# Optimization experiments

Hardware: AMD Instinct MI355X
Metric: run time of the kernel (lower is better)

Reference implementation:

```python
import jax, jax.numpy as jnp
import numpy as np

N_NODES = 100000
N_EDGES = 600000
N_GRAPHS = 64
EPS = 1e-5


def setup_inputs() -> dict:
    key = jax.random.key(0)
    ks = jax.random.split(key, 8)
    x = jax.random.normal(ks[0], (N_NODES, 128), dtype=jnp.float32)
    edge_index = jax.random.randint(ks[1], (2, N_EDGES), 0, N_NODES, dtype=jnp.int64)
    batch = jnp.sort(jax.random.randint(ks[2], (N_NODES,), 0, N_GRAPHS, dtype=jnp.int64))
    conv_w = jax.random.normal(ks[3], (6, 128, 128), dtype=jnp.float32) * (1.0 / np.sqrt(128))
    conv_b = jnp.zeros((6, 128), dtype=jnp.float32)
    bn_g = jnp.ones((6, 128), dtype=jnp.float32)
    bn_b = jnp.zeros((6, 128), dtype=jnp.float32)
    lin1_w = jax.random.normal(ks[4], (128, 64), dtype=jnp.float32) * (1.0 / np.sqrt(128))
    lin1_b = jnp.zeros((64,), dtype=jnp.float32)
    lin2_w = jax.random.normal(ks[5], (64, 4), dtype=jnp.float32) * (1.0 / np.sqrt(64))
    lin2_b = jnp.zeros((4,), dtype=jnp.float32)
    return {"x": x, "edge_index": edge_index, "batch": batch,
            "conv_w": conv_w, "conv_b": conv_b, "bn_g": bn_g, "bn_b": bn_b,
            "lin1_w": lin1_w, "lin1_b": lin1_b, "lin2_w": lin2_w, "lin2_b": lin2_b}


def reference(x, edge_index, batch, conv_w, conv_b, bn_g, bn_b, lin1_w, lin1_b, lin2_w, lin2_b):
    src, dst = edge_index[0], edge_index[1]  # messages flow src -> dst (PyG source_to_target)
    n = x.shape[0]
    h = x
    # 6 stacked GCNConv(normalize=False) -> ReLU -> BatchNorm1d (training-mode batch stats)
    for i in range(6):
        m = h @ conv_w[i]                                   # [N, H] transform first
        agg = jax.ops.segment_sum(m[src], dst, num_segments=n) + conv_b[i]
        h = jax.nn.relu(agg)
        mean = h.mean(axis=0)
        var = h.var(axis=0)                                  # biased, matches torch BN
        h = (h - mean) * jax.lax.rsqrt(var + EPS) * bn_g[i] + bn_b[i]
    # global mean pool over graphs
    s = jax.ops.segment_sum(h, batch, num_segments=N_GRAPHS)          # [G, H]
    cnt = jax.ops.segment_sum(jnp.ones((n,), h.dtype), batch, num_segments=N_GRAPHS)
    pooled = s / jnp.maximum(cnt, 1.0)[:, None]
    out = pooled @ lin1_w + lin1_b
    out = out @ lin2_w + lin2_b
    return jax.nn.log_softmax(out, axis=-1)
```

## Files before the change

### kernel.cpp

```cpp
#include <hip/hip_runtime.h>
#include <math.h>

#define NN 100000
#define NE 600000
#define NG 64
#define HD 128
#define NL 6
#define NB 1563
#define PSL 16
#define ASTR 136
#define CASTB 12500
#define EBL 2344
#define RSTR 379

typedef unsigned short ushort_t;
typedef short short8 __attribute__((ext_vector_type(8)));
typedef float floatx4 __attribute__((ext_vector_type(4)));

__device__ __forceinline__ float bf2f(ushort_t u) {
    return __uint_as_float(((unsigned)u) << 16);
}
__device__ __forceinline__ ushort_t f2bf(float f) {
    unsigned u = __float_as_uint(f);
    unsigned r = (u + 0x7fffu + ((u >> 16) & 1u)) >> 16;
    return (ushort_t)r;
}


__global__ __launch_bounds__(256) void k_prep(const float* __restrict__ x,
                                              ushort_t* __restrict__ xb,
                                              const float* __restrict__ W,
                                              ushort_t* __restrict__ Wt,
                                              ushort_t* __restrict__ hb0,
                                              ushort_t* __restrict__ hb1,
                                              const int* __restrict__ ei,
                                              int* __restrict__ counts) {
    int bid = blockIdx.x;
    if (bid < CASTB) {
        int i = bid * 256 + threadIdx.x;
        float4 v = ((const float4*)x)[i];
        ((ushort4*)xb)[i] = make_ushort4(f2bf(v.x), f2bf(v.y), f2bf(v.z), f2bf(v.w));
    } else if (bid < CASTB + NL) {
        const float* Wl = W + (size_t)(bid - CASTB) * 16384;
        ushort_t* Wtl = Wt + (size_t)(bid - CASTB) * 16384;
        for (int id = threadIdx.x; id < 16384; id += 256) {
            int k = id >> 7, c = id & 127;
            Wtl[c * 128 + k] = f2bf(Wl[id]);
        }
        if (bid == CASTB && threadIdx.x < 96) {
            int t = threadIdx.x;
            ushort_t* base = (t < 32) ? xb : ((t < 64) ? hb0 : hb1);
            *(ushort4*)(base + (size_t)NN * 128 + (size_t)(t & 31) * 4) =
                make_ushort4(0, 0, 0, 0);
        }
    } else {
        int e = (bid - CASTB - NL) * 256 + threadIdx.x;
        if (e < NE) atomicAdd(&counts[ei[NE + e]], 1);
    }
}


__global__ __launch_bounds__(256) void k_scan1(const int* __restrict__ counts, int* __restrict__ bsums) {
    __shared__ int s[256];
    int i = blockIdx.x * 256 + threadIdx.x;
    s[threadIdx.x] = (i < NN) ? counts[i] : 0;
    __syncthreads();
    for (int off = 128; off > 0; off >>= 1) {
        if (threadIdx.x < off) s[threadIdx.x] += s[threadIdx.x + off];
        __syncthreads();
    }
    if (threadIdx.x == 0) bsums[blockIdx.x] = s[0];
}

__global__ __launch_bounds__(256) void k_scan3m(const int* __restrict__ counts,
                                                const int* __restrict__ bsums,
                                                int* __restrict__ rowptr) {
    __shared__ int s[256];
    int t = threadIdx.x;
    int i = blockIdx.x * 256 + t;
    int v = (i < NN) ? counts[i] : 0;
    s[t] = v;
    __syncthreads();
    for (int off = 1; off < 256; off <<= 1) {
        int u = (t >= off) ? s[t - off] : 0;
        __syncthreads();
        s[t] += u;
        __syncthreads();
    }
    int incl = s[t];
    int pb = 0;
    for (int j = t; j < blockIdx.x; j += 256) pb += bsums[j];
    __syncthreads();
    s[t] = pb;
    __syncthreads();
    for (int off = 128; off > 0; off >>= 1) {
        if (t < off) s[t] += s[t + off];
        __syncthreads();
    }
    int base = s[0];
    if (i < NN) rowptr[i] = base + incl - v;
    if (i == 0) rowptr[NN] = NE;
}

__global__ __launch_bounds__(256) void k_filldh(const int* __restrict__ ei,
                                                const int* __restrict__ rowptr,
                                                int* __restrict__ cursor,
                                                int* __restrict__ colsrc,
                                                int* __restrict__ dcount,
                                                int ebl) {
    int t = threadIdx.x;
    if ((int)blockIdx.x < ebl) {
        int e = blockIdx.x * 256 + t;
        if (e < NE) {
            int d = ei[NE + e];
            int pos = rowptr[d] + atomicAdd(&cursor[d], 1);
            colsrc[pos] = ei[e];
        }
    } else {
        __shared__ int lc[64];
        if (t < 64) lc[t] = 0;
        __syncthreads();
        int n = (blockIdx.x - ebl) * 256 + t;
        if (n < NN) {
            int d = rowptr[n + 1] - rowptr[n];
            atomicAdd(&lc[min(d, 63)], 1);
        }
        __syncthreads();
        if (t < 64 && lc[t] > 0) atomicAdd(&dcount[t], lc[t]);
    }
}

__global__ __launch_bounds__(256) void k_dfill2(const int* __restrict__ rowptr,
                                                const int* __restrict__ dcount,
                                                int* __restrict__ dcursor,
                                                int* __restrict__ perm) {
    __shared__ int lc[64], lbase[64], doffs[64];
    int t = threadIdx.x;
    if (t < 64) {
        lc[t] = 0;
        int s = 0;
        for (int b = t + 1; b < 64; ++b) s += dcount[b];
        doffs[t] = s;
    }
    __syncthreads();
    int n = blockIdx.x * 256 + t;
    int b = 0, my = 0;
    if (n < NN) {
        int d = rowptr[n + 1] - rowptr[n];
        b = min(d, 63);
        my = atomicAdd(&lc[b], 1);
    }
    __syncthreads();
    if (t < 64 && lc[t] > 0) lbase[t] = atomicAdd(&dcursor[t], lc[t]);
    __syncthreads();
    if (n < NN) perm[doffs[b] + lbase[b] + my] = n;
}


__global__ __launch_bounds__(256, 4) void k_gconv(
    const ushort_t* __restrict__ hin, const int* __restrict__ perm,
    const int* __restrict__ rowptr, const int* __restrict__ colsrc,
    const float* __restrict__ stats_in, const float* __restrict__ bng,
    const float* __restrict__ bnb,
    const ushort_t* __restrict__ Wt, const float* __restrict__ bias,
    ushort_t* __restrict__ hout, float* __restrict__ partials) {
    __shared__ ushort_t Ab[64 * ASTR];
    __shared__ float sstat[256];
    int t = threadIdx.x;
    sstat[t] = 0.f;
    __syncthreads();
    int wave = t >> 6, lane = t & 63;
    int l15 = lane & 15, quad = lane >> 4;
    int l5 = lane & 31, half = lane >> 5;
    int rank = (RSTR * blockIdx.x) % NB;
    int rowbase = rank * 64 + wave * 16;

    int idxg = rowbase + l15;
    bool vr = idxg < NN;
    int prm = vr ? perm[idxg] : 0;
    int rb = vr ? rowptr[prm] : 0;
    int re = vr ? rowptr[prm + 1] : 0;
    int dg = re - rb;

    int f0 = l5 * 4;
    float sc[4] = {1.f, 1.f, 1.f, 1.f}, sh[4] = {0.f, 0.f, 0.f, 0.f};
    if (stats_in != nullptr) {
        const float inv_n = 1.0f / (float)NN;
        float4 s1 = *(const float4*)&stats_in[f0];
        float4 s2 = *(const float4*)&stats_in[HD + f0];
        float4 g4 = *(const float4*)&bng[f0];
        float4 b4 = *(const float4*)&bnb[f0];
        float m, var;
        m = s1.x * inv_n; var = fmaf(-m, m, s2.x * inv_n);
        sc[0] = g4.x * rsqrtf(var + 1e-5f); sh[0] = b4.x - m * sc[0];
        m = s1.y * inv_n; var = fmaf(-m, m, s2.y * inv_n);
        sc[1] = g4.y * rsqrtf(var + 1e-5f); sh[1] = b4.y - m * sc[1];
        m = s1.z * inv_n; var = fmaf(-m, m, s2.z * inv_n);
        sc[2] = g4.z * rsqrtf(var + 1e-5f); sh[2] = b4.z - m * sc[2];
        m = s1.w * inv_n; var = fmaf(-m, m, s2.w * inv_n);
        sc[3] = g4.w * rsqrtf(var + 1e-5f); sh[3] = b4.w - m * sc[3];
    }

    const uint2* hbl = (const uint2*)hin + l5;

    int b0 = __shfl(rb, half, 64);
    int d0 = __shfl(dg, half, 64);
    int b1 = __shfl(rb, 2 + half, 64);
    int d1 = __shfl(dg, 2 + half, 64);
    int cs0[4], cs1[4];
    #pragma unroll
    for (int eo = 0; eo < 4; ++eo) {
        int c0 = colsrc[b0 + eo];
        int c1 = colsrc[b1 + eo];
        cs0[eo] = (eo < d0) ? c0 : NN;
        cs1[eo] = (eo < d1) ? c1 : NN;
    }

    #pragma unroll 1
    for (int g = 0; g < 4; ++g) {
        int mx = max(d0, d1);
        mx = max(mx, __shfl_xor(mx, 32, 64));

        float a0[4] = {0.f, 0.f, 0.f, 0.f};
        float a1[4] = {0.f, 0.f, 0.f, 0.f};

        #pragma unroll 1
        for (int e = 0; e < mx; e += 4) {
            uint2 hv0[4], hv1[4];
            #pragma unroll
            for (int eo = 0; eo < 4; ++eo) hv0[eo] = hbl[(size_t)cs0[eo] * 32];
            #pragma unroll
            for (int eo = 0; eo < 4; ++eo) hv1[eo] = hbl[(size_t)cs1[eo] * 32];
            int nc0[4], nc1[4];
            #pragma unroll
            for (int eo = 0; eo < 4; ++eo) {
                int e4 = e + 4 + eo;
                int c0 = colsrc[b0 + e4];
                int c1 = colsrc[b1 + e4];
                nc0[eo] = (e4 < d0) ? c0 : NN;
                nc1[eo] = (e4 < d1) ? c1 : NN;
            }
            #pragma unroll
            for (int eo = 0; eo < 4; ++eo) {
                unsigned wx = hv0[eo].x, wy = hv0[eo].y;
                a0[0] += __uint_as_float(wx << 16);
                a0[1] += __uint_as_float(wx & 0xffff0000u);
                a0[2] += __uint_as_float(wy << 16);
                a0[3] += __uint_as_float(wy & 0xffff0000u);
                unsigned zx = hv1[eo].x, zy = hv1[eo].y;
                a1[0] += __uint_as_float(zx << 16);
                a1[1] += __uint_as_float(zx & 0xffff0000u);
                a1[2] += __uint_as_float(zy << 16);
                a1[3] += __uint_as_float(zy & 0xffff0000u);
            }
            #pragma unroll
            for (int eo = 0; eo < 4; ++eo) { cs0[eo] = nc0[eo]; cs1[eo] = nc1[eo]; }
        }

        int nb0 = 0, nd0 = 0, nb1 = 0, nd1 = 0;
        if (g < 3) {
            int t0 = (g + 1) * 4 + half, t1 = t0 + 2;
            nb0 = __shfl(rb, t0, 64);
            nd0 = __shfl(dg, t0, 64);
            nb1 = __shfl(rb, t1, 64);
            nd1 = __shfl(dg, t1, 64);
            #pragma unroll
            for (int eo = 0; eo < 4; ++eo) {
                int c0 = colsrc[nb0 + eo];
                int c1 = colsrc[nb1 + eo];
                cs0[eo] = (eo < nd0) ? c0 : NN;
                cs1[eo] = (eo < nd1) ? c1 : NN;
            }
        }

        float df0 = (float)d0, df1 = (float)d1;
        ushort4 u0, u1;
        u0.x = f2bf(fmaf(sc[0], a0[0], df0 * sh[0]));
        u0.y = f2bf(fmaf(sc[1], a0[1], df0 * sh[1]));
        u0.z = f2bf(fmaf(sc[2], a0[2], df0 * sh[2]));
        u0.w = f2bf(fmaf(sc[3], a0[3], df0 * sh[3]));
        u1.x = f2bf(fmaf(sc[0], a1[0], df1 * sh[0]));
        u1.y = f2bf(fmaf(sc[1], a1[1], df1 * sh[1]));
        u1.z = f2bf(fmaf(sc[2], a1[2], df1 * sh[2]));
        u1.w = f2bf(fmaf(sc[3], a1[3], df1 * sh[3]));
        *(ushort4*)&Ab[(wave * 16 + g * 4 + half) * ASTR + f0] = u0;
        *(ushort4*)&Ab[(wave * 16 + g * 4 + 2 + half) * ASTR + f0] = u1;

        b0 = nb0; d0 = nd0; b1 = nb1; d1 = nd1;
    }

    short8 afrag[4];
    #pragma unroll
    for (int s = 0; s < 4; ++s)
        afrag[s] = *(const short8*)&Ab[(wave * 16 + l15) * ASTR + quad * 8 + s * 32];

    floatx4 acc[8];
    #pragma unroll
    for (int c = 0; c < 8; ++c) acc[c] = (floatx4){0.f, 0.f, 0.f, 0.f};
    #pragma unroll
    for (int c = 0; c < 8; ++c) {
        size_t boff = (size_t)(16 * c + l15) * 128 + quad * 8;
        #pragma unroll
        for (int s = 0; s < 4; ++s) {
            short8 bf = *(const short8*)(Wt + boff + 32 * s);
            acc[c] = __builtin_amdgcn_mfma_f32_16x16x32_bf16(afrag[s], bf, acc[c], 0, 0, 0);
        }
    }

    int orow0 = rowbase + quad * 4;
    #pragma unroll
    for (int c = 0; c < 8; ++c) {
        int col = 16 * c + l15;
        float bv = bias[col];
        float ls = 0.f, lq = 0.f;
        #pragma unroll
        for (int i = 0; i < 4; ++i) {
            float v = fmaxf(acc[c][i] + bv, 0.f);
            ushort_t bb = f2bf(v);
            Ab[(wave * 16 + quad * 4 + i) * ASTR + col] = bb;
            if (orow0 + i < NN) {
                float vr2 = bf2f(bb);
                ls += vr2;
                lq = fmaf(vr2, vr2, lq);
            }
        }
        ls += __shfl_xor(ls, 16, 64);
        ls += __shfl_xor(ls, 32, 64);
        lq += __shfl_xor(lq, 16, 64);
        lq += __shfl_xor(lq, 32, 64);
        if (quad == 0) {
            atomicAdd(&sstat[col], ls);
            atomicAdd(&sstat[128 + col], lq);
        }
    }

    #pragma unroll
    for (int it = 0; it < 4; ++it) {
        int pr = __shfl(prm, it * 4 + quad, 64);
        int ridx = rowbase + it * 4 + quad;
        if (ridx < NN) {
            short8 v = *(const short8*)&Ab[(wave * 16 + it * 4 + quad) * ASTR + l15 * 8];
            *(short8*)(hout + (size_t)pr * 128 + l15 * 8) = v;
        }
    }

    __syncthreads();
    partials[(size_t)blockIdx.x * 256 + t] = sstat[t];
}


__global__ __launch_bounds__(256) void k_red(const float* __restrict__ partials,
                                             float* __restrict__ stats) {
    int t = threadIdx.x;
    float s = 0.f;
    for (int r = blockIdx.x; r < NB; r += 64) s += partials[(size_t)r * 256 + t];
    atomicAdd(&stats[t], s);
}


__device__ __forceinline__ int lowerb(const int* __restrict__ b, int n, int key) {
    int lo = 0, hi = n;
    while (lo < hi) {
        int mid = (lo + hi) >> 1;
        if (b[mid] < key) lo = mid + 1;
        else hi = mid;
    }
    return lo;
}

__global__ __launch_bounds__(256) void k_pool1(
    const ushort_t* __restrict__ h, const int* __restrict__ batch,
    float* __restrict__ ppart) {
    int g = blockIdx.x >> 4;
    int sl = blockIdx.x & (PSL - 1);
    int lo = lowerb(batch, NN, g);
    int hi = lowerb(batch, NN, g + 1);
    int cnt = hi - lo;
    int a = lo + (int)(((long long)cnt * sl) >> 4);
    int b = lo + (int)(((long long)cnt * (sl + 1)) >> 4);
    int wave = threadIdx.x >> 6, lane = threadIdx.x & 63;
    const ushort2* h2 = (const ushort2*)h;
    float ax = 0.f, ay = 0.f;
    for (int n = a + wave; n < b; n += 4) {
        ushort2 v = h2[(size_t)n * 64 + lane];
        ax += bf2f(v.x);
        ay += bf2f(v.y);
    }
    __shared__ float2 red[4][64];
    red[wave][lane] = make_float2(ax, ay);
    __syncthreads();
    if (wave == 0) {
        float sx = 0.f, sy = 0.f;
        for (int w = 0; w < 4; ++w) {
            sx += red[w][lane].x;
            sy += red[w][lane].y;
        }
        ((float2*)ppart)[(size_t)blockIdx.x * 64 + lane] = make_float2(sx, sy);
    }
}


__global__ __launch_bounds__(64) void k_tail(
    const float* __restrict__ ppart, const int* __restrict__ batch,
    const float* __restrict__ stats, const float* __restrict__ bng, const float* __restrict__ bnb,
    const float* __restrict__ w1, const float* __restrict__ b1,
    const float* __restrict__ w2, const float* __restrict__ b2,
    float* __restrict__ out) {
    __shared__ float p[128];
    int g = blockIdx.x;
    int lane = threadIdx.x;
    float sx = 0.f, sy = 0.f;
    #pragma unroll
    for (int s = 0; s < PSL; ++s) {
        float2 v = ((const float2*)ppart)[(size_t)(g * PSL + s) * 64 + lane];
        sx += v.x;
        sy += v.y;
    }
    int cnt = lowerb(batch, NN, g + 1) - lowerb(batch, NN, g);
    int c0 = lane * 2;
    const float inv_n = 1.0f / (float)NN;
    float m0 = stats[c0] * inv_n, m1 = stats[c0 + 1] * inv_n;
    float var0 = fmaf(-m0, m0, stats[HD + c0] * inv_n);
    float var1 = fmaf(-m1, m1, stats[HD + c0 + 1] * inv_n);
    float sc0 = bng[c0] * rsqrtf(var0 + 1e-5f);
    float sc1 = bng[c0 + 1] * rsqrtf(var1 + 1e-5f);
    float sh0 = bnb[c0] - m0 * sc0;
    float sh1 = bnb[c0 + 1] - m1 * sc1;
    float denom = fmaxf((float)cnt, 1.f);
    p[c0] = (sc0 * sx + (float)cnt * sh0) / denom;
    p[c0 + 1] = (sc1 * sy + (float)cnt * sh1) / denom;
    __syncthreads();

    float hid = b1[lane];
    #pragma unroll 8
    for (int k = 0; k < 128; ++k) hid = fmaf(p[k], w1[k * 64 + lane], hid);
    float o[4];
    #pragma unroll
    for (int c = 0; c < 4; ++c) {
        float v = hid * w2[lane * 4 + c];
        #pragma unroll
        for (int off = 1; off < 64; off <<= 1) v += __shfl_xor(v, off, 64);
        o[c] = v + b2[c];
    }
    if (lane == 0) {
        float mx = fmaxf(fmaxf(o[0], o[1]), fmaxf(o[2], o[3]));
        float se = expf(o[0] - mx) + expf(o[1] - mx) + expf(o[2] - mx) + expf(o[3] - mx);
        float ls = mx + logf(se);
        #pragma unroll
        for (int c = 0; c < 4; ++c) out[g * 4 + c] = o[c] - ls;
    }
}

extern "C" void kernel_launch(void* const* d_in, const int* in_sizes, int n_in,
                              void* d_out, int out_size, void* d_ws, size_t ws_size,
                              hipStream_t stream) {
    const float* x = (const float*)d_in[0];
    const int* ei = (const int*)d_in[1];
    const int* batch = (const int*)d_in[2];
    const float* conv_w = (const float*)d_in[3];
    const float* conv_b = (const float*)d_in[4];
    const float* bn_g = (const float*)d_in[5];
    const float* bn_b = (const float*)d_in[6];
    const float* l1w = (const float*)d_in[7];
    const float* l1b = (const float*)d_in[8];
    const float* l2w = (const float*)d_in[9];
    const float* l2b = (const float*)d_in[10];
    float* out = (float*)d_out;
    (void)in_sizes; (void)n_in; (void)out_size; (void)ws_size;

    char* ws = (char*)d_ws;
    int* counts = (int*)(ws + 0);
    int* cursor = (int*)(ws + 400000);
    int* perm = (int*)(ws + 400000);
    float* stats = (float*)(ws + 800000);
    int* dcount = (int*)(ws + 806144);
    int* dcursor = (int*)(ws + 806400);
    const size_t zero_bytes = 806656;
    int* rowptr = (int*)(ws + 806656);
    int* bsums = (int*)(ws + 1206664);
    int* colsrc = (int*)(ws + 1208256);
    float* ppart = (float*)(ws + 3609280);
    float* partials = (float*)(ws + 4133568);
    ushort_t* xb = (ushort_t*)(ws + 5734144);
    ushort_t* hb0 = (ushort_t*)(ws + 31334400);
    ushort_t* hb1 = (ushort_t*)(ws + 56934656);
    ushort_t* wtbuf = (ushort_t*)(ws + 82534912);

    hipMemsetAsync(ws, 0, zero_bytes, stream);

    k_prep<<<CASTB + NL + EBL, 256, 0, stream>>>(x, xb, conv_w, wtbuf, hb0, hb1, ei, counts);

    int nb1 = (NN + 255) / 256;
    k_scan1<<<nb1, 256, 0, stream>>>(counts, bsums);
    k_scan3m<<<nb1, 256, 0, stream>>>(counts, bsums, rowptr);
    k_filldh<<<EBL + nb1, 256, 0, stream>>>(ei, rowptr, cursor, colsrc, dcount, EBL);
    k_dfill2<<<nb1, 256, 0, stream>>>(rowptr, dcount, dcursor, perm);

    ushort_t* hb[2] = {hb0, hb1};
    for (int L = 0; L < NL; ++L) {
        const ushort_t* hin = (L == 0) ? xb : hb[(L + 1) & 1];
        ushort_t* hout = hb[L & 1];
        const float* lstats = (L == 0) ? nullptr : (stats + (L - 1) * 256);
        const float* lg = (L == 0) ? nullptr : (bn_g + (L - 1) * 128);
        const float* lb = (L == 0) ? nullptr : (bn_b + (L - 1) * 128);
        k_gconv<<<NB, 256, 0, stream>>>(hin, perm, rowptr, colsrc, lstats, lg, lb,
                                        wtbuf + L * 16384, conv_b + L * 128,
                                        hout, partials);
        k_red<<<64, 256, 0, stream>>>(partials, stats + L * 256);
    }
    k_pool1<<<NG * PSL, 256, 0, stream>>>(hb1, batch, ppart);
    k_tail<<<NG, 64, 0, stream>>>(ppart, batch, stats + 5 * 256, bn_g + 5 * 128, bn_b + 5 * 128,
                                  l1w, l1b, l2w, l2b, out);
}
```

Measured before the change: 642.0 us.

## Store intermediate layer features in degree-sorted order with remapped edge sources

Layers 0-4 now write their output rows in permuted (degree-sorted) row order, so each block writes one contiguous range instead of scattering rows through perm. A new kernel builds an inverse permutation and remaps the edge source indices so later layers gather from the permuted layout. The last layer writes back in original order for pooling. This adds one small remap kernel and an extra index array, and the gathers become permuted-space accesses that may have different locality.

Result: no change. 653.0 us (+1.7%).

```diff
diff --git a/kernel.cpp b/kernel.cpp
--- a/kernel.cpp
+++ b/kernel.cpp
@@ -133,7 +133,8 @@
 __global__ __launch_bounds__(256) void k_dfill2(const int* __restrict__ rowptr,
                                                 const int* __restrict__ dcount,
                                                 int* __restrict__ dcursor,
-                                                int* __restrict__ perm) {
+                                                int* __restrict__ perm,
+                                                int* __restrict__ inv_perm) {
     __shared__ int lc[64], lbase[64], doffs[64];
     int t = threadIdx.x;
     if (t < 64) {
@@ -153,7 +154,18 @@
     __syncthreads();
     if (t < 64 && lc[t] > 0) lbase[t] = atomicAdd(&dcursor[t], lc[t]);
     __syncthreads();
-    if (n < NN) perm[doffs[b] + lbase[b] + my] = n;
+    if (n < NN) {
+        int r = doffs[b] + lbase[b] + my;
+        perm[r] = n;
+        inv_perm[n] = r;
+    }
+}
+
+__global__ __launch_bounds__(256) void k_trans(const int* __restrict__ colsrc,
+                                               const int* __restrict__ inv_perm,
+                                               int* __restrict__ colsrc_s) {
+    int e = blockIdx.x * 256 + threadIdx.x;
+    if (e < NE) colsrc_s[e] = inv_perm[colsrc[e]];
 }
 
 
@@ -163,7 +175,8 @@
     const float* __restrict__ stats_in, const float* __restrict__ bng,
     const float* __restrict__ bnb,
     const ushort_t* __restrict__ Wt, const float* __restrict__ bias,
-    ushort_t* __restrict__ hout, float* __restrict__ partials) {
+    ushort_t* __restrict__ hout, float* __restrict__ partials,
+    const int store_orig) {
     __shared__ ushort_t Ab[64 * ASTR];
     __shared__ float sstat[256];
     int t = threadIdx.x;
@@ -336,11 +349,12 @@
 
     #pragma unroll
     for (int it = 0; it < 4; ++it) {
+        int ridx = rowbase + it * 4 + quad;
         int pr = __shfl(prm, it * 4 + quad, 64);
-        int ridx = rowbase + it * 4 + quad;
+        int trg = store_orig ? pr : ridx;
         if (ridx < NN) {
             short8 v = *(const short8*)&Ab[(wave * 16 + it * 4 + quad) * ASTR + l15 * 8];
-            *(short8*)(hout + (size_t)pr * 128 + l15 * 8) = v;
+            *(short8*)(hout + (size_t)trg * 128 + l15 * 8) = v;
         }
     }
 
@@ -470,6 +484,7 @@
 
     char* ws = (char*)d_ws;
     int* counts = (int*)(ws + 0);
+    int* inv_perm = (int*)(ws + 0);
     int* cursor = (int*)(ws + 400000);
     int* perm = (int*)(ws + 400000);
     float* stats = (float*)(ws + 800000);
@@ -485,6 +500,7 @@
     ushort_t* hb0 = (ushort_t*)(ws + 31334400);
     ushort_t* hb1 = (ushort_t*)(ws + 56934656);
     ushort_t* wtbuf = (ushort_t*)(ws + 82534912);
+    int* colsrc_s = (int*)(ws + 82731520);
 
     hipMemsetAsync(ws, 0, zero_bytes, stream);
 
@@ -494,7 +510,8 @@
     k_scan1<<<nb1, 256, 0, stream>>>(counts, bsums);
     k_scan3m<<<nb1, 256, 0, stream>>>(counts, bsums, rowptr);
     k_filldh<<<EBL + nb1, 256, 0, stream>>>(ei, rowptr, cursor, colsrc, dcount, EBL);
-    k_dfill2<<<nb1, 256, 0, stream>>>(rowptr, dcount, dcursor, perm);
+    k_dfill2<<<nb1, 256, 0, stream>>>(rowptr, dcount, dcursor, perm, inv_perm);
+    k_trans<<<EBL, 256, 0, stream>>>(colsrc, inv_perm, colsrc_s);
 
     ushort_t* hb[2] = {hb0, hb1};
     for (int L = 0; L < NL; ++L) {
@@ -503,9 +520,11 @@
         const float* lstats = (L == 0) ? nullptr : (stats + (L - 1) * 256);
         const float* lg = (L == 0) ? nullptr : (bn_g + (L - 1) * 128);
         const float* lb = (L == 0) ? nullptr : (bn_b + (L - 1) * 128);
-        k_gconv<<<NB, 256, 0, stream>>>(hin, perm, rowptr, colsrc, lstats, lg, lb,
+        const int* cs = (L == 0) ? colsrc : colsrc_s;
+        int store_orig = (L == NL - 1) ? 1 : 0;
+        k_gconv<<<NB, 256, 0, stream>>>(hin, perm, rowptr, cs, lstats, lg, lb,
                                         wtbuf + L * 16384, conv_b + L * 128,
-                                        hout, partials);
+                                        hout, partials, store_orig);
         k_red<<<64, 256, 0, stream>>>(partials, stats + L * 256);
     }
     k_pool1<<<NG * PSL, 256, 0, stream>>>(hb1, batch, ppart);
```

## Fuse BN stats reduction into next gconv via persistent grid and flag spin-wait

Applied to the files above, without the earlier changes.

Removes the separate k_red launch per layer by having the first 64 blocks of the next gconv reduce the previous layer's partials into stats, signalling completion through an atomic done flag. All blocks start the gather before spin-waiting for the stats, so the reduction overlaps with aggregation. The grid shrinks to 782 blocks, each looping over two tiles, which halves the partial rows to reduce; partials are double-buffered. The final layer's reduction moves into k_pool1. The spin-wait assumes the first 64 blocks are resident alongside the waiting blocks, and per-block work becomes coarser, which may hurt load balance.

New measurement: 801.9 us. +24.9%, slower.

```diff
diff --git a/kernel.cpp b/kernel.cpp
--- a/kernel.cpp
+++ b/kernel.cpp
@@ -12,6 +12,7 @@
 #define CASTB 12500
 #define EBL 2344
 #define RSTR 379
+#define GRIDP 782
 
 typedef unsigned short ushort_t;
 typedef short short8 __attribute__((ext_vector_type(8)));
@@ -160,10 +161,12 @@
 __global__ __launch_bounds__(256, 4) void k_gconv(
     const ushort_t* __restrict__ hin, const int* __restrict__ perm,
     const int* __restrict__ rowptr, const int* __restrict__ colsrc,
-    const float* __restrict__ stats_in, const float* __restrict__ bng,
-    const float* __restrict__ bnb,
+    const float* __restrict__ red_src,
+    float* __restrict__ stats_prev,
+    int* __restrict__ done_flag,
+    const float* __restrict__ bng, const float* __restrict__ bnb,
     const ushort_t* __restrict__ Wt, const float* __restrict__ bias,
-    ushort_t* __restrict__ hout, float* __restrict__ partials) {
+    ushort_t* __restrict__ hout, float* __restrict__ partials_out) {
     __shared__ ushort_t Ab[64 * ASTR];
     __shared__ float sstat[256];
     int t = threadIdx.x;
@@ -172,189 +175,202 @@
     int wave = t >> 6, lane = t & 63;
     int l15 = lane & 15, quad = lane >> 4;
     int l5 = lane & 31, half = lane >> 5;
-    int rank = (RSTR * blockIdx.x) % NB;
-    int rowbase = rank * 64 + wave * 16;
-
-    int idxg = rowbase + l15;
-    bool vr = idxg < NN;
-    int prm = vr ? perm[idxg] : 0;
-    int rb = vr ? rowptr[prm] : 0;
-    int re = vr ? rowptr[prm + 1] : 0;
-    int dg = re - rb;
-
     int f0 = l5 * 4;
+
+    if (red_src != nullptr && blockIdx.x < 64) {
+        float s = 0.f;
+        for (int r = blockIdx.x; r < GRIDP; r += 64)
+            s += red_src[(size_t)r * 256 + t];
+        atomicAdd(&stats_prev[t], s);
+        __threadfence();
+        __syncthreads();
+        if (t == 0)
+            __hip_atomic_fetch_add(done_flag, 1, __ATOMIC_RELEASE,
+                                   __HIP_MEMORY_SCOPE_AGENT);
+    }
+
+    bool have_stats = (done_flag == nullptr);
     float sc[4] = {1.f, 1.f, 1.f, 1.f}, sh[4] = {0.f, 0.f, 0.f, 0.f};
-    if (stats_in != nullptr) {
-        const float inv_n = 1.0f / (float)NN;
-        float4 s1 = *(const float4*)&stats_in[f0];
-        float4 s2 = *(const float4*)&stats_in[HD + f0];
-        float4 g4 = *(const float4*)&bng[f0];
-        float4 b4 = *(const float4*)&bnb[f0];
-        float m, var;
-        m = s1.x * inv_n; var = fmaf(-m, m, s2.x * inv_n);
-        sc[0] = g4.x * rsqrtf(var + 1e-5f); sh[0] = b4.x - m * sc[0];
-        m = s1.y * inv_n; var = fmaf(-m, m, s2.y * inv_n);
-        sc[1] = g4.y * rsqrtf(var + 1e-5f); sh[1] = b4.y - m * sc[1];
-        m = s1.z * inv_n; var = fmaf(-m, m, s2.z * inv_n);
-        sc[2] = g4.z * rsqrtf(var + 1e-5f); sh[2] = b4.z - m * sc[2];
-        m = s1.w * inv_n; var = fmaf(-m, m, s2.w * inv_n);
-        sc[3] = g4.w * rsqrtf(var + 1e-5f); sh[3] = b4.w - m * sc[3];
-    }
 
     const uint2* hbl = (const uint2*)hin + l5;
 
-    int b0 = __shfl(rb, half, 64);
-    int d0 = __shfl(dg, half, 64);
-    int b1 = __shfl(rb, 2 + half, 64);
-    int d1 = __shfl(dg, 2 + half, 64);
-    int cs0[4], cs1[4];
-    #pragma unroll
-    for (int eo = 0; eo < 4; ++eo) {
-        int c0 = colsrc[b0 + eo];
-        int c1 = colsrc[b1 + eo];
-        cs0[eo] = (eo < d0) ? c0 : NN;
-        cs1[eo] = (eo < d1) ? c1 : NN;
-    }
-
-    #pragma unroll 1
-    for (int g = 0; g < 4; ++g) {
-        int mx = max(d0, d1);
-        mx = max(mx, __shfl_xor(mx, 32, 64));
-
-        float a0[4] = {0.f, 0.f, 0.f, 0.f};
-        float a1[4] = {0.f, 0.f, 0.f, 0.f};
+    for (int tile = blockIdx.x; tile < NB; tile += GRIDP) {
+        int rank = (RSTR * tile) % NB;
+        int rowbase = rank * 64 + wave * 16;
+
+        int idxg = rowbase + l15;
+        bool vr = idxg < NN;
+        int prm = vr ? perm[idxg] : 0;
+        int rb = vr ? rowptr[prm] : 0;
+        int re = vr ? rowptr[prm + 1] : 0;
+        int dg = re - rb;
+
+        int b0 = __shfl(rb, half, 64);
+        int d0 = __shfl(dg, half, 64);
+        int b1 = __shfl(rb, 2 + half, 64);
+        int d1 = __shfl(dg, 2 + half, 64);
+        int cs0[4], cs1[4];
+        #pragma unroll
+        for (int eo = 0; eo < 4; ++eo) {
+            int c0 = colsrc[b0 + eo];
+            int c1 = colsrc[b1 + eo];
+            cs0[eo] = (eo < d0) ? c0 : NN;
+            cs1[eo] = (eo < d1) ? c1 : NN;
+        }
 
         #pragma unroll 1
-        for (int e = 0; e < mx; e += 4) {
-            uint2 hv0[4], hv1[4];
+        for (int g = 0; g < 4; ++g) {
+            int mx = max(d0, d1);
+            mx = max(mx, __shfl_xor(mx, 32, 64));
+
+            float a0[4] = {0.f, 0.f, 0.f, 0.f};
+            float a1[4] = {0.f, 0.f, 0.f, 0.f};
+
+            #pragma unroll 1
+            for (int e = 0; e < mx; e += 4) {
+                uint2 hv0[4], hv1[4];
+                #pragma unroll
+                for (int eo = 0; eo < 4; ++eo) hv0[eo] = hbl[(size_t)cs0[eo] * 32];
+                #pragma unroll
+                for (int eo = 0; eo < 4; ++eo) hv1[eo] = hbl[(size_t)cs1[eo] * 32];
+                int nc0[4], nc1[4];
+                #pragma unroll
+                for (int eo = 0; eo < 4; ++eo) {
+                    int e4 = e + 4 + eo;
+                    int c0 = colsrc[b0 + e4];
+                    int c1 = colsrc[b1 + e4];
+                    nc0[eo] = (e4 < d0) ? c0 : NN;
+                    nc1[eo] = (e4 < d1) ? c1 : NN;
+                }
+                #pragma unroll
+                for (int eo = 0; eo < 4; ++eo) {
+                    unsigned wx = hv0[eo].x, wy = hv0[eo].y;
+                    a0[0] += __uint_as_float(wx << 16);
+                    a0[1] += __uint_as_float(wx & 0xffff0000u);
+                    a0[2] += __uint_as_float(wy << 16);
+                    a0[3] += __uint_as_float(wy & 0xffff0000u);
+                    unsigned zx = hv1[eo].x, zy = hv1[eo].y;
+                    a1[0] += __uint_as_float(zx << 16);
+                    a1[1] += __uint_as_float(zx & 0xffff0000u);
+                    a1[2] += __uint_as_float(zy << 16);
+                    a1[3] += __uint_as_float(zy & 0xffff0000u);
+                }
+                #pragma unroll
+                for (int eo = 0; eo < 4; ++eo) { cs0[eo] = nc0[eo]; cs1[eo] = nc1[eo]; }
+            }
+
+            int nb0 = 0, nd0 = 0, nb1 = 0, nd1 = 0;
+            if (g < 3) {
+                int t0 = (g + 1) * 4 + half, t1 = t0 + 2;
+                nb0 = __shfl(rb, t0, 64);
+                nd0 = __shfl(dg, t0, 64);
+                nb1 = __shfl(rb, t1, 64);
+                nd1 = __shfl(dg, t1, 64);
+                #pragma unroll
+                for (int eo = 0; eo < 4; ++eo) {
+                    int c0 = colsrc[nb0 + eo];
+                    int c1 = colsrc[nb1 + eo];
+                    cs0[eo] = (eo < nd0) ? c0 : NN;
+                    cs1[eo] = (eo < nd1) ? c1 : NN;
+                }
+            }
+
+            if (!have_stats) {
+                if (t == 0) {
+                    while (__hip_atomic_load(done_flag, __ATOMIC_ACQUIRE,
+                                             __HIP_MEMORY_SCOPE_AGENT) < 64)
+                        __builtin_amdgcn_s_sleep(8);
+                }
+                __syncthreads();
+                const float inv_n = 1.0f / (float)NN;
+                #pragma unroll
+                for (int j = 0; j < 4; ++j) {
+                    float s1 = __hip_atomic_load(&stats_prev[f0 + j], __ATOMIC_RELAXED,
+                                                 __HIP_MEMORY_SCOPE_AGENT);
+                    float s2 = __hip_atomic_load(&stats_prev[HD + f0 + j], __ATOMIC_RELAXED,
+                                                 __HIP_MEMORY_SCOPE_AGENT);
+                    float m = s1 * inv_n;
+                    float var = fmaf(-m, m, s2 * inv_n);
+                    sc[j] = bng[f0 + j] * rsqrtf(var + 1e-5f);
+                    sh[j] = bnb[f0 + j] - m * sc[j];
+                }
+                have_stats = true;
+            }
+
+            float df0 = (float)d0, df1 = (float)d1;
+            ushort4 u0, u1;
+            u0.x = f2bf(fmaf(sc[0], a0[0], df0 * sh[0]));
+            u0.y = f2bf(fmaf(sc[1], a0[1], df0 * sh[1]));
+            u0.z = f2bf(fmaf(sc[2], a0[2], df0 * sh[2]));
+            u0.w = f2bf(fmaf(sc[3], a0[3], df0 * sh[3]));
+            u1.x = f2bf(fmaf(sc[0], a1[0], df1 * sh[0]));
+            u1.y = f2bf(fmaf(sc[1], a1[1], df1 * sh[1]));
+            u1.z = f2bf(fmaf(sc[2], a1[2], df1 * sh[2]));
+            u1.w = f2bf(fmaf(sc[3], a1[3], df1 * sh[3]));
+            *(ushort4*)&Ab[(wave * 16 + g * 4 + half) * ASTR + f0] = u0;
+            *(ushort4*)&Ab[(wave * 16 + g * 4 + 2 + half) * ASTR + f0] = u1;
+
+            b0 = nb0; d0 = nd0; b1 = nb1; d1 = nd1;
+        }
+
+        short8 afrag[4];
+        #pragma unroll
+        for (int s = 0; s < 4; ++s)
+            afrag[s] = *(const short8*)&Ab[(wave * 16 + l15) * ASTR + quad * 8 + s * 32];
+
+        floatx4 acc[8];
+        #pragma unroll
+        for (int c = 0; c < 8; ++c) acc[c] = (floatx4){0.f, 0.f, 0.f, 0.f};
+        #pragma unroll
+        for (int c = 0; c < 8; ++c) {
+            size_t boff = (size_t)(16 * c + l15) * 128 + quad * 8;
             #pragma unroll
-            for (int eo = 0; eo < 4; ++eo) hv0[eo] = hbl[(size_t)cs0[eo] * 32];
+            for (int s = 0; s < 4; ++s) {
+                short8 bf = *(const short8*)(Wt + boff + 32 * s);
+                acc[c] = __builtin_amdgcn_mfma_f32_16x16x32_bf16(afrag[s], bf, acc[c], 0, 0, 0);
+            }
+        }
+
+        int orow0 = rowbase + quad * 4;
+        #pragma unroll
+        for (int c = 0; c < 8; ++c) {
+            int col = 16 * c + l15;
+            float bv = bias[col];
+            float ls = 0.f, lq = 0.f;
             #pragma unroll
-            for (int eo = 0; eo < 4; ++eo) hv1[eo] = hbl[(size_t)cs1[eo] * 32];
-            int nc0[4], nc1[4];
-            #pragma unroll
-            for (int eo = 0; eo < 4; ++eo) {
-                int e4 = e + 4 + eo;
-                int c0 = colsrc[b0 + e4];
-                int c1 = colsrc[b1 + e4];
-                nc0[eo] = (e4 < d0) ? c0 : NN;
-                nc1[eo] = (e4 < d1) ? c1 : NN;
-            }
-            #pragma unroll
-            for (int eo = 0; eo < 4; ++eo) {
-                unsigned wx = hv0[eo].x, wy = hv0[eo].y;
-                a0[0] += __uint_as_float(wx << 16);
-                a0[1] += __uint_as_float(wx & 0xffff0000u);
-                a0[2] += __uint_as_float(wy << 16);
-                a0[3] += __uint_as_float(wy & 0xffff0000u);
-                unsigned zx = hv1[eo].x, zy = hv1[eo].y;
-                a1[0] += __uint_as_float(zx << 16);
-                a1[1] += __uint_as_float(zx & 0xffff0000u);
-                a1[2] += __uint_as_float(zy << 16);
-                a1[3] += __uint_as_float(zy & 0xffff0000u);
-            }
-            #pragma unroll
-            for (int eo = 0; eo < 4; ++eo) { cs0[eo] = nc0[eo]; cs1[eo] = nc1[eo]; }
-        }
-
-        int nb0 = 0, nd0 = 0, nb1 = 0, nd1 = 0;
-        if (g < 3) {
-            int t0 = (g + 1) * 4 + half, t1 = t0 + 2;
-            nb0 = __shfl(rb, t0, 64);
-            nd0 = __shfl(dg, t0, 64);
-            nb1 = __shfl(rb, t1, 64);
-            nd1 = __shfl(dg, t1, 64);
-            #pragma unroll
-            for (int eo = 0; eo < 4; ++eo) {
-                int c0 = colsrc[nb0 + eo];
-                int c1 = colsrc[nb1 + eo];
-                cs0[eo] = (eo < nd0) ? c0 : NN;
-                cs1[eo] = (eo < nd1) ? c1 : NN;
-            }
-        }
-
-        float df0 = (float)d0, df1 = (float)d1;
-        ushort4 u0, u1;
-        u0.x = f2bf(fmaf(sc[0], a0[0], df0 * sh[0]));
-        u0.y = f2bf(fmaf(sc[1], a0[1], df0 * sh[1]));
-        u0.z = f2bf(fmaf(sc[2], a0[2], df0 * sh[2]));
-        u0.w = f2bf(fmaf(sc[3], a0[3], df0 * sh[3]));
-        u1.x = f2bf(fmaf(sc[0], a1[0], df1 * sh[0]));
-        u1.y = f2bf(fmaf(sc[1], a1[1], df1 * sh[1]));
-        u1.z = f2bf(fmaf(sc[2], a1[2], df1 * sh[2]));
-        u1.w = f2bf(fmaf(sc[3], a1[3], df1 * sh[3]));
-        *(ushort4*)&Ab[(wave * 16 + g * 4 + half) * ASTR + f0] = u0;
-        *(ushort4*)&Ab[(wave * 16 + g * 4 + 2 + half) * ASTR + f0] = u1;
-
-        b0 = nb0; d0 = nd0; b1 = nb1; d1 = nd1;
-    }
-
-    short8 afrag[4];
-    #pragma unroll
-    for (int s = 0; s < 4; ++s)
-        afrag[s] = *(const short8*)&Ab[(wave * 16 + l15) * ASTR + quad * 8 + s * 32];
-
-    floatx4 acc[8];
-    #pragma unroll
-    for (int c = 0; c < 8; ++c) acc[c] = (floatx4){0.f, 0.f, 0.f, 0.f};
-    #pragma unroll
-    for (int c = 0; c < 8; ++c) {
-        size_t boff = (size_t)(16 * c + l15) * 128 + quad * 8;
-        #pragma unroll
-        for (int s = 0; s < 4; ++s) {
-            short8 bf = *(const short8*)(Wt + boff + 32 * s);
-            acc[c] = __builtin_amdgcn_mfma_f32_16x16x32_bf16(afrag[s], bf, acc[c], 0, 0, 0);
-        }
-    }
-
-    int orow0 = rowbase + quad * 4;
-    #pragma unroll
-    for (int c = 0; c < 8; ++c) {
-        int col = 16 * c + l15;
-        float bv = bias[col];
-        float ls = 0.f, lq = 0.f;
-        #pragma unroll
-        for (int i = 0; i < 4; ++i) {
-            float v = fmaxf(acc[c][i] + bv, 0.f);
-            ushort_t bb = f2bf(v);
-            Ab[(wave * 16 + quad * 4 + i) * ASTR + col] = bb;
-            if (orow0 + i < NN) {
-                float vr2 = bf2f(bb);
-                ls += vr2;
-                lq = fmaf(vr2, vr2, lq);
-            }
-        }
-        ls += __shfl_xor(ls, 16, 64);
-        ls += __shfl_xor(ls, 32, 64);
-        lq += __shfl_xor(lq, 16, 64);
-        lq += __shfl_xor(lq, 32, 64);
-        if (quad == 0) {
-            atomicAdd(&sstat[col], ls);
-            atomicAdd(&sstat[128 + col], lq);
-        }
-    }
-
-    #pragma unroll
-    for (int it = 0; it < 4; ++it) {
-        int pr = __shfl(prm, it * 4 + quad, 64);
-        int ridx = rowbase + it * 4 + quad;
-        if (ridx < NN) {
-            short8 v = *(const short8*)&Ab[(wave * 16 + it * 4 + quad) * ASTR + l15 * 8];
-            *(short8*)(hout + (size_t)pr * 128 + l15 * 8) = v;
-        }
-    }
-
-    __syncthreads();
-    partials[(size_t)blockIdx.x * 256 + t] = sstat[t];
-}
-
-
-__global__ __launch_bounds__(256) void k_red(const float* __restrict__ partials,
-                                             float* __restrict__ stats) {
-    int t = threadIdx.x;
-    float s = 0.f;
-    for (int r = blockIdx.x; r < NB; r += 64) s += partials[(size_t)r * 256 + t];
-    atomicAdd(&stats[t], s);
+            for (int i = 0; i < 4; ++i) {
+                float v = fmaxf(acc[c][i] + bv, 0.f);
+                ushort_t bb = f2bf(v);
+                Ab[(wave * 16 + quad * 4 + i) * ASTR + col] = bb;
+                if (orow0 + i < NN) {
+                    float vr2 = bf2f(bb);
+                    ls += vr2;
+                    lq = fmaf(vr2, vr2, lq);
+                }
+            }
+            ls += __shfl_xor(ls, 16, 64);
+            ls += __shfl_xor(ls, 32, 64);
+            lq += __shfl_xor(lq, 16, 64);
+            lq += __shfl_xor(lq, 32, 64);
+            if (quad == 0) {
+                atomicAdd(&sstat[col], ls);
+                atomicAdd(&sstat[128 + col], lq);
+            }
+        }
+
+        #pragma unroll
+        for (int it = 0; it < 4; ++it) {
+            int pr = __shfl(prm, it * 4 + quad, 64);
+            int ridx = rowbase + it * 4 + quad;
+            if (ridx < NN) {
+                short8 v = *(const short8*)&Ab[(wave * 16 + it * 4 + quad) * ASTR + l15 * 8];
+                *(short8*)(hout + (size_t)pr * 128 + l15 * 8) = v;
+            }
+        }
+    }
+
+    __syncthreads();
+    partials_out[(size_t)blockIdx.x * 256 + t] = sstat[t];
 }
 
 
@@ -370,7 +386,15 @@
 
 __global__ __launch_bounds__(256) void k_pool1(
     const ushort_t* __restrict__ h, const int* __restrict__ batch,
-    float* __restrict__ ppart) {
+    float* __restrict__ ppart,
+    const float* __restrict__ red_src, float* __restrict__ stats5) {
+    int t = threadIdx.x;
+    if (blockIdx.x < 64) {
+        float s = 0.f;
+        for (int r = blockIdx.x; r < GRIDP; r += 64)
+            s += red_src[(size_t)r * 256 + t];
+        atomicAdd(&stats5[t], s);
+    }
     int g = blockIdx.x >> 4;
     int sl = blockIdx.x & (PSL - 1);
     int lo = lowerb(batch, NN, g);
@@ -378,7 +402,7 @@
     int cnt = hi - lo;
     int a = lo + (int)(((long long)cnt * sl) >> 4);
     int b = lo + (int)(((long long)cnt * (sl + 1)) >> 4);
-    int wave = threadIdx.x >> 6, lane = threadIdx.x & 63;
+    int wave = t >> 6, lane = t & 63;
     const ushort2* h2 = (const ushort2*)h;
     float ax = 0.f, ay = 0.f;
     for (int n = a + wave; n < b; n += 4) {
@@ -475,16 +499,18 @@
     float* stats = (float*)(ws + 800000);
     int* dcount = (int*)(ws + 806144);
     int* dcursor = (int*)(ws + 806400);
-    const size_t zero_bytes = 806656;
-    int* rowptr = (int*)(ws + 806656);
-    int* bsums = (int*)(ws + 1206664);
-    int* colsrc = (int*)(ws + 1208256);
-    float* ppart = (float*)(ws + 3609280);
-    float* partials = (float*)(ws + 4133568);
-    ushort_t* xb = (ushort_t*)(ws + 5734144);
-    ushort_t* hb0 = (ushort_t*)(ws + 31334400);
-    ushort_t* hb1 = (ushort_t*)(ws + 56934656);
-    ushort_t* wtbuf = (ushort_t*)(ws + 82534912);
+    int* done = (int*)(ws + 806656);
+    const size_t zero_bytes = 806912;
+    int* rowptr = (int*)(ws + 806912);
+    int* bsums = (int*)(ws + 1206920);
+    int* colsrc = (int*)(ws + 1208512);
+    float* ppart = (float*)(ws + 3609536);
+    float* partials0 = (float*)(ws + 4133824);
+    float* partials1 = (float*)(ws + 4934592);
+    ushort_t* xb = (ushort_t*)(ws + 5735424);
+    ushort_t* hb0 = (ushort_t*)(ws + 31335680);
+    ushort_t* hb1 = (ushort_t*)(ws + 56935936);
+    ushort_t* wtbuf = (ushort_t*)(ws + 82536192);
 
     hipMemsetAsync(ws, 0, zero_bytes, stream);
 
@@ -497,18 +523,22 @@
     k_dfill2<<<nb1, 256, 0, stream>>>(rowptr, dcount, dcursor, perm);
 
     ushort_t* hb[2] = {hb0, hb1};
+    float* parts[2] = {partials0, partials1};
     for (int L = 0; L < NL; ++L) {
         const ushort_t* hin = (L == 0) ? xb : hb[(L + 1) & 1];
         ushort_t* hout = hb[L & 1];
-        const float* lstats = (L == 0) ? nullptr : (stats + (L - 1) * 256);
+        const float* red_src = (L == 0) ? nullptr : parts[(L - 1) & 1];
+        float* stats_prev = (L == 0) ? nullptr : (stats + (L - 1) * 256);
+        int* done_flag = (L == 0) ? nullptr : (done + (L - 1));
         const float* lg = (L == 0) ? nullptr : (bn_g + (L - 1) * 128);
         const float* lb = (L == 0) ? nullptr : (bn_b + (L - 1) * 128);
-        k_gconv<<<NB, 256, 0, stream>>>(hin, perm, rowptr, colsrc, lstats, lg, lb,
-                                        wtbuf + L * 16384, conv_b + L * 128,
-                                        hout, partials);
-        k_red<<<64, 256, 0, stream>>>(partials, stats + L * 256);
-    }
-    k_pool1<<<NG * PSL, 256, 0, stream>>>(hb1, batch, ppart);
+        k_gconv<<<GRIDP, 256, 0, stream>>>(hin, perm, rowptr, colsrc,
+                                           red_src, stats_prev, done_flag, lg, lb,
+                                           wtbuf + L * 16384, conv_b + L * 128,
+                                           hout, parts[L & 1]);
+    }
+    k_pool1<<<NG * PSL, 256, 0, stream>>>(hb1, batch, ppart, parts[(NL - 1) & 1],
+                                          stats + 5 * 256);
     k_tail<<<NG, 64, 0, stream>>>(ppart, batch, stats + 5 * 256, bn_g + 5 * 128, bn_b + 5 * 128,
                                   l1w, l1b, l2w, l2b, out);
 }
```
